# Performance work log

Measured on AMD Instinct MI355X. Metric: run time of the kernel, lower is better.

## Reference

```python
import jax, jax.numpy as jnp
import numpy as np

N = 100000   # nodes
E = 640000   # edges
G = 256      # graphs in batch
H = 128      # hidden_dim
OUT = 128    # output_dim
IN = 1       # input_dim ('standard' encoding)


def _linear_init(k, din, dout):
    # torch nn.Linear default: U(-1/sqrt(din), 1/sqrt(din)) for weight and bias
    s = 1.0 / np.sqrt(din)
    kw, kb = jax.random.split(k)
    W = jax.random.uniform(kw, (din, dout), jnp.float32, -s, s)
    b = jax.random.uniform(kb, (dout,), jnp.float32, -s, s)
    return W, b


def setup_inputs() -> dict:
    key = jax.random.key(0)
    ks = jax.random.split(key, 10)
    x = jax.random.normal(ks[0], (N, IN), jnp.float32)
    edge_index = jax.random.randint(ks[1], (2, E), 0, N, dtype=jnp.int64)
    batch = jnp.sort(jax.random.randint(ks[2], (N,), 0, G, dtype=jnp.int64))
    inp = {"x": x, "edge_index": edge_index, "batch": batch}
    dims_in = [IN, H, H]  # layer 0 takes input_dim, rest take hidden_dim
    i = 3
    for l, din in enumerate(dims_in):
        inp[f"W1_{l}"], inp[f"b1_{l}"] = _linear_init(ks[i], din, H); i += 1
        inp[f"W2_{l}"], inp[f"b2_{l}"] = _linear_init(ks[i], H, H); i += 1
    inp["Wfc"], inp["bfc"] = _linear_init(ks[i], H, OUT)
    return inp


def reference(x, edge_index, batch,
              W1_0, b1_0, W2_0, b2_0,
              W1_1, b1_1, W2_1, b2_1,
              W1_2, b1_2, W2_2, b2_2,
              Wfc, bfc):
    src, dst = edge_index[0], edge_index[1]

    def gin_conv(h, W1, b1, W2, b2):
        # GINConv, eps=0: out = MLP(h + sum_{j->i} h_j)
        agg = jax.ops.segment_sum(h[src], dst, num_segments=N)  # scatter-add messages
        z = h + agg
        return jnp.maximum(z @ W1 + b1, 0.0) @ W2 + b2

    h = gin_conv(x, W1_0, b1_0, W2_0, b2_0)
    h = gin_conv(h, W1_1, b1_1, W2_1, b2_1)
    h = gin_conv(h, W1_2, b1_2, W2_2, b2_2)
    pooled = jax.ops.segment_sum(h, batch, num_segments=G)  # global_add_pool -> [G, H]
    return pooled @ Wfc + bfc  # [G, OUT]
```

## Files before the change

### kernel.cpp

```cpp
#include <hip/hip_runtime.h>

#define HH 128
#define GG 256
#define CAP 32
#define PSPLIT 16

using f32x4  = __attribute__((ext_vector_type(4))) float;
using bf16x4 = __attribute__((ext_vector_type(4))) __bf16;
using bf16x8 = __attribute__((ext_vector_type(8))) __bf16;

static __device__ __forceinline__ float bf2f(unsigned int u) {
    unsigned int x = u << 16;
    return __builtin_bit_cast(float, x);
}
static __device__ __forceinline__ unsigned short f2bf(float f) {
    __bf16 b = (__bf16)f;
    return __builtin_bit_cast(unsigned short, b);
}

__global__ __launch_bounds__(256) void prep_k(
    int* __restrict__ cnt, float* __restrict__ pooled, int n,
    const float* __restrict__ Wa, const float* __restrict__ Wb,
    const float* __restrict__ Wc, const float* __restrict__ Wd,
    const float* __restrict__ We, __bf16* __restrict__ Wp,
    const int* __restrict__ batch, int* __restrict__ bound, int zb)
{
    const int t = threadIdx.x, b = blockIdx.x;
    if (b < zb) {
        const int i = b * 256 + t;
        if (i < n) cnt[i] = 0;
        if (i < GG * HH) pooled[i] = 0.f;
    } else if (b < zb + 40) {
        const int which = b - zb;
        const int mat = which >> 3;
        const float* W = (mat == 0) ? Wa : (mat == 1) ? Wb : (mat == 2) ? Wc
                       : (mat == 3) ? Wd : We;
        const int slot = (which & 7) * 256 + t;
        const int frag = slot >> 6, lane = slot & 63;
        const int mb = frag >> 2, kb = frag & 3;
        const int col = mb * 16 + (lane & 15);
        const int k0  = kb * 32 + (lane >> 4) * 8;
        bf16x8 v;
        #pragma unroll
        for (int j = 0; j < 8; ++j) v[j] = (__bf16)W[(k0 + j) * HH + col];
        *(bf16x8*)&Wp[(size_t)mat * 16384 + slot * 8] = v;
    } else {
        const int g = t;
        int lo = 0, hi = n;
        while (lo < hi) { int m = (lo + hi) >> 1; if (batch[m] < g) lo = m + 1; else hi = m; }
        bound[g] = lo;
        if (g == 0) bound[GG] = n;
    }
}

__global__ __launch_bounds__(256) void fill_k(const int* __restrict__ src,
                                              const int* __restrict__ dst,
                                              int* __restrict__ cnt,
                                              int* __restrict__ slotbuf, int ne)
{
    int e = blockIdx.x * 256 + threadIdx.x;
    if (e < ne) {
        const int d = dst[e];
        const int off = atomicAdd(&cnt[d], 1);
        if (off < CAP) slotbuf[d * CAP + off] = src[e];
    }
}

__global__ __launch_bounds__(256) void l0_k(
    const float* __restrict__ x,
    const int* __restrict__ cnt, const int* __restrict__ slotbuf,
    const float* __restrict__ W1, const float* __restrict__ b1,
    const __bf16* __restrict__ Wp2, const float* __restrict__ b2,
    unsigned short* __restrict__ hout, int n)
{
    __shared__ __bf16 Wl[16384];
    __shared__ unsigned short tt[4][4096];
    __shared__ float b1l[HH], b2l[HH], w1l[HH];

    const int t    = threadIdx.x;
    const int lane = t & 63, wv = t >> 6;
    const int l16  = lane & 15, lq = lane >> 4;
    const int r0    = blockIdx.x * 128 + wv * 32;
    const int nodeA = r0 + l16, nodeB = r0 + 16 + l16;
    const int rowA  = min(nodeA, n - 1), rowB = min(nodeB, n - 1);
    const int swz   = (l16 & 7) << 4;

    #pragma unroll
    for (int i = 0; i < 8; ++i)
        *(int4*)&Wl[(i * 256 + t) * 8] = *(const int4*)&Wp2[(i * 256 + t) * 8];
    if (t < HH) { b2l[t] = b2[t]; b1l[t] = b1[t]; w1l[t] = W1[t]; }

    float sA, sB;
    {
        float s0 = x[rowA], s1 = 0.f, s2 = 0.f, s3 = 0.f;
        const int dA = min(cnt[rowA], CAP);
        const int* sp = &slotbuf[rowA * CAP];
        for (int j = 0; j < dA; j += 4) {
            const int i1 = min(j + 1, dA - 1), i2 = min(j + 2, dA - 1), i3 = min(j + 3, dA - 1);
            const float v0 = x[sp[j]],  v1 = x[sp[i1]];
            const float v2 = x[sp[i2]], v3 = x[sp[i3]];
            s0 += v0;
            s1 += (j + 1 < dA) ? v1 : 0.f;
            s2 += (j + 2 < dA) ? v2 : 0.f;
            s3 += (j + 3 < dA) ? v3 : 0.f;
        }
        sA = (s0 + s1) + (s2 + s3);
        s0 = x[rowB]; s1 = s2 = s3 = 0.f;
        const int dB = min(cnt[rowB], CAP);
        const int* sq = &slotbuf[rowB * CAP];
        for (int j = 0; j < dB; j += 4) {
            const int i1 = min(j + 1, dB - 1), i2 = min(j + 2, dB - 1), i3 = min(j + 3, dB - 1);
            const float v0 = x[sq[j]],  v1 = x[sq[i1]];
            const float v2 = x[sq[i2]], v3 = x[sq[i3]];
            s0 += v0;
            s1 += (j + 1 < dB) ? v1 : 0.f;
            s2 += (j + 2 < dB) ? v2 : 0.f;
            s3 += (j + 3 < dB) ? v3 : 0.f;
        }
        sB = (s0 + s1) + (s2 + s3);
    }
    __syncthreads();

    char* tl = (char*)tt[wv];
    #pragma unroll
    for (int mt = 0; mt < 8; ++mt) {
        const f32x4 w  = *(const f32x4*)&w1l[mt * 16 + lq * 4];
        const f32x4 bb = *(const f32x4*)&b1l[mt * 16 + lq * 4];
        bf16x4 pa, pb;
        #pragma unroll
        for (int r = 0; r < 4; ++r) {
            pa[r] = (__bf16)fmaxf(fmaf(sA, w[r], bb[r]), 0.f);
            pb[r] = (__bf16)fmaxf(fmaf(sB, w[r], bb[r]), 0.f);
        }
        *(bf16x4*)(tl + ((l16 * 256 + mt * 32 + lq * 8) ^ swz)) = pa;
        *(bf16x4*)(tl + (((16 + l16) * 256 + mt * 32 + lq * 8) ^ swz)) = pb;
    }
    __syncthreads();

    bf16x8 tfA[4], tfB[4];
    #pragma unroll
    for (int kb = 0; kb < 4; ++kb) {
        tfA[kb] = *(const bf16x8*)(tl + ((l16 * 256 + kb * 64 + lq * 16) ^ swz));
        tfB[kb] = *(const bf16x8*)(tl + (((16 + l16) * 256 + kb * 64 + lq * 16) ^ swz));
    }
    f32x4 a2A[8], a2B[8];
    #pragma unroll
    for (int mb = 0; mb < 8; ++mb) {
        const f32x4 bb = *(const f32x4*)&b2l[mb * 16 + lq * 4];
        a2A[mb] = bb; a2B[mb] = bb;
    }
    #pragma unroll
    for (int mb = 0; mb < 8; ++mb)
        #pragma unroll
        for (int kb = 0; kb < 4; ++kb) {
            const bf16x8 wf = *(const bf16x8*)&Wl[((mb * 4 + kb) * 64 + lane) * 8];
            a2A[mb] = __builtin_amdgcn_mfma_f32_16x16x32_bf16(wf, tfA[kb], a2A[mb], 0, 0, 0);
            a2B[mb] = __builtin_amdgcn_mfma_f32_16x16x32_bf16(wf, tfB[kb], a2B[mb], 0, 0, 0);
        }
    if (nodeA < n) {
        #pragma unroll
        for (int mb = 0; mb < 8; ++mb) {
            bf16x4 p;
            #pragma unroll
            for (int r = 0; r < 4; ++r) p[r] = (__bf16)a2A[mb][r];
            *(bf16x4*)&hout[(size_t)nodeA * HH + mb * 16 + lq * 4] = p;
        }
    }
    if (nodeB < n) {
        #pragma unroll
        for (int mb = 0; mb < 8; ++mb) {
            bf16x4 p;
            #pragma unroll
            for (int r = 0; r < 4; ++r) p[r] = (__bf16)a2B[mb][r];
            *(bf16x4*)&hout[(size_t)nodeB * HH + mb * 16 + lq * 4] = p;
        }
    }
}

static __device__ __forceinline__ void agg_body(
    const unsigned short* __restrict__ h, const int* __restrict__ cnt,
    const int* __restrict__ slotbuf, unsigned short* __restrict__ z, int n)
{
    const int wave = (blockIdx.x * 256 + threadIdx.x) >> 6;
    const int lane = threadIdx.x & 63;
    const int half = lane >> 5, sl = lane & 31;
    const int nw   = (gridDim.x * 256) >> 6;
    const int npairs = (n + 1) >> 1;
    const uint2* h8 = (const uint2*)h;
    uint2* z8 = (uint2*)z;

    for (int pr = wave; pr < npairs; pr += nw) {
        const int node = min(2 * pr + half, n - 1);
        const int deg = min(cnt[node], CAP);
        const int* sp = &slotbuf[node * CAP];
        const uint2 su = h8[(size_t)node * 32 + sl];
        float a0 = bf2f(su.x & 0xffff), a1 = bf2f(su.x >> 16);
        float a2 = bf2f(su.y & 0xffff), a3 = bf2f(su.y >> 16);
        float b0 = 0.f, b1 = 0.f, b2 = 0.f, b3 = 0.f;
        float c0 = 0.f, c1 = 0.f, c2 = 0.f, c3 = 0.f;
        float d0 = 0.f, d1 = 0.f, d2 = 0.f, d3 = 0.f;
        for (int j = 0; j < deg; j += 4) {
            const int i1 = min(j + 1, deg - 1), i2 = min(j + 2, deg - 1), i3 = min(j + 3, deg - 1);
            const uint2 v0 = h8[(size_t)sp[j]  * 32 + sl];
            const uint2 v1 = h8[(size_t)sp[i1] * 32 + sl];
            const uint2 v2 = h8[(size_t)sp[i2] * 32 + sl];
            const uint2 v3 = h8[(size_t)sp[i3] * 32 + sl];
            a0 += bf2f(v0.x & 0xffff); a1 += bf2f(v0.x >> 16);
            a2 += bf2f(v0.y & 0xffff); a3 += bf2f(v0.y >> 16);
            const bool m1 = (j + 1 < deg), m2 = (j + 2 < deg), m3 = (j + 3 < deg);
            b0 += m1 ? bf2f(v1.x & 0xffff) : 0.f; b1 += m1 ? bf2f(v1.x >> 16) : 0.f;
            b2 += m1 ? bf2f(v1.y & 0xffff) : 0.f; b3 += m1 ? bf2f(v1.y >> 16) : 0.f;
            c0 += m2 ? bf2f(v2.x & 0xffff) : 0.f; c1 += m2 ? bf2f(v2.x >> 16) : 0.f;
            c2 += m2 ? bf2f(v2.y & 0xffff) : 0.f; c3 += m2 ? bf2f(v2.y >> 16) : 0.f;
            d0 += m3 ? bf2f(v3.x & 0xffff) : 0.f; d1 += m3 ? bf2f(v3.x >> 16) : 0.f;
            d2 += m3 ? bf2f(v3.y & 0xffff) : 0.f; d3 += m3 ? bf2f(v3.y >> 16) : 0.f;
        }
        const float s0 = (a0 + b0) + (c0 + d0);
        const float s1 = (a1 + b1) + (c1 + d1);
        const float s2 = (a2 + b2) + (c2 + d2);
        const float s3 = (a3 + b3) + (c3 + d3);
        uint2 o;
        o.x = (unsigned int)f2bf(s0) | ((unsigned int)f2bf(s1) << 16);
        o.y = (unsigned int)f2bf(s2) | ((unsigned int)f2bf(s3) << 16);
        z8[(size_t)node * 32 + sl] = o;
    }
}
__global__ __launch_bounds__(256) void agg1_k(const unsigned short* h, const int* cnt,
                                              const int* slotbuf, unsigned short* z, int n)
{ agg_body(h, cnt, slotbuf, z, n); }
__global__ __launch_bounds__(256) void agg2_k(const unsigned short* h, const int* cnt,
                                              const int* slotbuf, unsigned short* z, int n)
{ agg_body(h, cnt, slotbuf, z, n); }

static __device__ __forceinline__ void mlp_body8(
    const unsigned short* __restrict__ z,
    const __bf16* __restrict__ Wp1, const float* __restrict__ b1,
    const __bf16* __restrict__ Wp2, const float* __restrict__ b2,
    unsigned short* __restrict__ hout, int n)
{
    __shared__ __bf16 Wl1[16384], Wl2[16384];
    __shared__ unsigned short tt[8][4096];
    __shared__ float b1l[HH], b2l[HH];

    const int t    = threadIdx.x;
    const int lane = t & 63, wv = t >> 6;
    const int l16  = lane & 15, lq = lane >> 4;
    const int r0    = blockIdx.x * 256 + wv * 32;
    const int nodeA = r0 + l16, nodeB = r0 + 16 + l16;
    const int rowA  = min(nodeA, n - 1), rowB = min(nodeB, n - 1);
    const int swz   = (l16 & 7) << 4;

    #pragma unroll
    for (int i = 0; i < 4; ++i) {
        *(int4*)&Wl1[(i * 512 + t) * 8] = *(const int4*)&Wp1[(i * 512 + t) * 8];
        *(int4*)&Wl2[(i * 512 + t) * 8] = *(const int4*)&Wp2[(i * 512 + t) * 8];
    }
    if (t < HH) b1l[t] = b1[t];
    else if (t < 2 * HH) b2l[t - HH] = b2[t - HH];

    bf16x8 zfA[4], zfB[4];
    #pragma unroll
    for (int kb = 0; kb < 4; ++kb) {
        zfA[kb] = *(const bf16x8*)&z[(size_t)rowA * HH + kb * 32 + lq * 8];
        zfB[kb] = *(const bf16x8*)&z[(size_t)rowB * HH + kb * 32 + lq * 8];
    }
    __syncthreads();

    f32x4 a1A[8], a1B[8];
    #pragma unroll
    for (int mt = 0; mt < 8; ++mt) {
        const f32x4 bb = *(const f32x4*)&b1l[mt * 16 + lq * 4];
        a1A[mt] = bb; a1B[mt] = bb;
    }
    #pragma unroll
    for (int mt = 0; mt < 8; ++mt)
        #pragma unroll
        for (int kb = 0; kb < 4; ++kb) {
            const bf16x8 wf = *(const bf16x8*)&Wl1[((mt * 4 + kb) * 64 + lane) * 8];
            a1A[mt] = __builtin_amdgcn_mfma_f32_16x16x32_bf16(wf, zfA[kb], a1A[mt], 0, 0, 0);
            a1B[mt] = __builtin_amdgcn_mfma_f32_16x16x32_bf16(wf, zfB[kb], a1B[mt], 0, 0, 0);
        }
    char* tl = (char*)tt[wv];
    #pragma unroll
    for (int mt = 0; mt < 8; ++mt) {
        bf16x4 pa, pb;
        #pragma unroll
        for (int r = 0; r < 4; ++r) {
            pa[r] = (__bf16)fmaxf(a1A[mt][r], 0.f);
            pb[r] = (__bf16)fmaxf(a1B[mt][r], 0.f);
        }
        *(bf16x4*)(tl + ((l16 * 256 + mt * 32 + lq * 8) ^ swz)) = pa;
        *(bf16x4*)(tl + (((16 + l16) * 256 + mt * 32 + lq * 8) ^ swz)) = pb;
    }
    __syncthreads();

    bf16x8 tfA[4], tfB[4];
    #pragma unroll
    for (int kb = 0; kb < 4; ++kb) {
        tfA[kb] = *(const bf16x8*)(tl + ((l16 * 256 + kb * 64 + lq * 16) ^ swz));
        tfB[kb] = *(const bf16x8*)(tl + (((16 + l16) * 256 + kb * 64 + lq * 16) ^ swz));
    }
    f32x4 a2A[8], a2B[8];
    #pragma unroll
    for (int mb = 0; mb < 8; ++mb) {
        const f32x4 bb = *(const f32x4*)&b2l[mb * 16 + lq * 4];
        a2A[mb] = bb; a2B[mb] = bb;
    }
    #pragma unroll
    for (int mb = 0; mb < 8; ++mb)
        #pragma unroll
        for (int kb = 0; kb < 4; ++kb) {
            const bf16x8 wf = *(const bf16x8*)&Wl2[((mb * 4 + kb) * 64 + lane) * 8];
            a2A[mb] = __builtin_amdgcn_mfma_f32_16x16x32_bf16(wf, tfA[kb], a2A[mb], 0, 0, 0);
            a2B[mb] = __builtin_amdgcn_mfma_f32_16x16x32_bf16(wf, tfB[kb], a2B[mb], 0, 0, 0);
        }

    if (nodeA < n) {
        #pragma unroll
        for (int mb = 0; mb < 8; ++mb) {
            bf16x4 p;
            #pragma unroll
            for (int r = 0; r < 4; ++r) p[r] = (__bf16)a2A[mb][r];
            *(bf16x4*)&hout[(size_t)nodeA * HH + mb * 16 + lq * 4] = p;
        }
    }
    if (nodeB < n) {
        #pragma unroll
        for (int mb = 0; mb < 8; ++mb) {
            bf16x4 p;
            #pragma unroll
            for (int r = 0; r < 4; ++r) p[r] = (__bf16)a2B[mb][r];
            *(bf16x4*)&hout[(size_t)nodeB * HH + mb * 16 + lq * 4] = p;
        }
    }
}

__global__ __launch_bounds__(512) void mlp1_k(const unsigned short* z,
                                              const __bf16* Wp1, const float* b1,
                                              const __bf16* Wp2, const float* b2,
                                              unsigned short* h, int n)
{ mlp_body8(z, Wp1, b1, Wp2, b2, h, n); }

__global__ __launch_bounds__(512) void mlp2_k(const unsigned short* z,
                                              const __bf16* Wp1, const float* b1,
                                              const __bf16* Wp2, const float* b2,
                                              unsigned short* h, int n)
{ mlp_body8(z, Wp1, b1, Wp2, b2, h, n); }

__global__ __launch_bounds__(64) void pool_k(const unsigned short* __restrict__ h,
                                             const int* __restrict__ bound,
                                             float* __restrict__ pooled)
{
    const int g = blockIdx.x >> 4;
    const int s = blockIdx.x & (PSPLIT - 1);
    const int t = threadIdx.x;
    const int half = t >> 5, sl = t & 31;
    const int rb = bound[g], re = bound[g + 1];
    const int len = re - rb;
    const int i0 = rb + (int)(((long)len * s) / PSPLIT);
    const int i1 = rb + (int)(((long)len * (s + 1)) / PSPLIT);
    const uint2* h8 = (const uint2*)h;

    float p0 = 0.f, p1 = 0.f, p2 = 0.f, p3 = 0.f;
    float q0 = 0.f, q1 = 0.f, q2 = 0.f, q3 = 0.f;
    int r = i0 + half;
    for (; r + 2 < i1; r += 4) {
        const uint2 a = h8[(size_t)r * 32 + sl];
        const uint2 b = h8[(size_t)(r + 2) * 32 + sl];
        p0 += bf2f(a.x & 0xffff); p1 += bf2f(a.x >> 16);
        p2 += bf2f(a.y & 0xffff); p3 += bf2f(a.y >> 16);
        q0 += bf2f(b.x & 0xffff); q1 += bf2f(b.x >> 16);
        q2 += bf2f(b.y & 0xffff); q3 += bf2f(b.y >> 16);
    }
    if (r < i1) {
        const uint2 a = h8[(size_t)r * 32 + sl];
        p0 += bf2f(a.x & 0xffff); p1 += bf2f(a.x >> 16);
        p2 += bf2f(a.y & 0xffff); p3 += bf2f(a.y >> 16);
    }
    p0 += q0; p1 += q1; p2 += q2; p3 += q3;
    if (i0 + half < i1) {
        float* p = &pooled[g * HH + sl * 4];
        unsafeAtomicAdd(p + 0, p0);
        unsafeAtomicAdd(p + 1, p1);
        unsafeAtomicAdd(p + 2, p2);
        unsafeAtomicAdd(p + 3, p3);
    }
}

__global__ __launch_bounds__(128) void fc_k(const float* __restrict__ pooled,
                                            const float* __restrict__ Wfc,
                                            const float* __restrict__ bfc,
                                            float* __restrict__ out)
{
    __shared__ float p[HH];
    const int g = blockIdx.x, k = threadIdx.x;
    p[k] = pooled[g * HH + k];
    __syncthreads();
    float acc = bfc[k];
    #pragma unroll 8
    for (int j = 0; j < HH; ++j) acc = fmaf(p[j], Wfc[j * HH + k], acc);
    out[g * HH + k] = acc;
}

extern "C" void kernel_launch(void* const* d_in, const int* in_sizes, int n_in,
                              void* d_out, int out_size, void* d_ws, size_t ws_size,
                              hipStream_t stream)
{
    const float* x     = (const float*)d_in[0];
    const int*   ei    = (const int*)d_in[1];
    const int*   batch = (const int*)d_in[2];
    const float* W1_0 = (const float*)d_in[3];
    const float* b1_0 = (const float*)d_in[4];
    const float* W2_0 = (const float*)d_in[5];
    const float* b2_0 = (const float*)d_in[6];
    const float* W1_1 = (const float*)d_in[7];
    const float* b1_1 = (const float*)d_in[8];
    const float* W2_1 = (const float*)d_in[9];
    const float* b2_1 = (const float*)d_in[10];
    const float* W1_2 = (const float*)d_in[11];
    const float* b1_2 = (const float*)d_in[12];
    const float* W2_2 = (const float*)d_in[13];
    const float* b2_2 = (const float*)d_in[14];
    const float* Wfc  = (const float*)d_in[15];
    const float* bfc  = (const float*)d_in[16];

    const int N = in_sizes[0];
    const int E = in_sizes[1] / 2;
    const int* src = ei;
    const int* dst = ei + E;

    char* p = (char*)d_ws;
    #define CARVE(ty, name, count) ty* name = (ty*)p; p += (((size_t)(count) * sizeof(ty)) + 255) & ~(size_t)255;
    CARVE(unsigned short, hA,     (size_t)N * HH)
    CARVE(unsigned short, hB,     (size_t)N * HH)
    CARVE(float,          pooled, GG * HH)
    CARVE(int,            cnt,    N)
    CARVE(int,            slotbuf,(size_t)N * CAP)
    CARVE(int,            bound,  GG + 1)
    CARVE(__bf16,         Wp,     5 * 16384)
    #undef CARVE
    float* outp = (float*)d_out;

    const int gblk  = (N + 127) / 128;
    const int gblk8 = (N + 255) / 256;
    const int zb    = (N + 255) / 256;

    prep_k<<<zb + 41, 256, 0, stream>>>(cnt, pooled, N, W2_0, W1_1, W2_1, W1_2, W2_2,
                                        Wp, batch, bound, zb);
    fill_k<<<(E + 255) / 256, 256, 0, stream>>>(src, dst, cnt, slotbuf, E);

    l0_k<<<gblk, 256, 0, stream>>>(x, cnt, slotbuf, W1_0, b1_0, Wp, b2_0, hA, N);

    agg1_k<<<2048, 256, 0, stream>>>(hA, cnt, slotbuf, hB, N);
    mlp1_k<<<gblk8, 512, 0, stream>>>(hB, Wp + 16384, b1_1, Wp + 2 * 16384, b2_1, hA, N);

    agg2_k<<<2048, 256, 0, stream>>>(hA, cnt, slotbuf, hB, N);
    mlp2_k<<<gblk8, 512, 0, stream>>>(hB, Wp + 3 * 16384, b1_2, Wp + 4 * 16384, b2_2, hA, N);

    pool_k<<<GG * PSPLIT, 64, 0, stream>>>(hA, bound, pooled);
    fc_k<<<GG, HH, 0, stream>>>(pooled, Wfc, bfc, outp);
}
```

Before: 206.2 us.

## Fuse global add pooling into final MLP epilogue with shuffle-reduced atomics

The last GIN layer's MLP kernel now accumulates its outputs straight into the pooled per-graph buffer instead of writing the hidden state to memory. When a 16-row tile lies entirely inside one graph, it reduces the tile with cross-lane shuffles and issues one atomic per column; otherwise it falls back to per-node atomics. This drops the separate pool kernel, the graph-boundary binary search in prep, and one full write and read of the N×128 bf16 hidden tensor. The cost is extra shuffles and float atomics in the MLP epilogue, and the pooled sums keep fp32 outputs without rounding them to bf16 first.

```diff
diff --git a/kernel.cpp b/kernel.cpp
--- a/kernel.cpp
+++ b/kernel.cpp
@@ -3,7 +3,6 @@
 #define HH 128
 #define GG 256
 #define CAP 32
-#define PSPLIT 16
 
 using f32x4  = __attribute__((ext_vector_type(4))) float;
 using bf16x4 = __attribute__((ext_vector_type(4))) __bf16;
@@ -22,15 +21,14 @@
     int* __restrict__ cnt, float* __restrict__ pooled, int n,
     const float* __restrict__ Wa, const float* __restrict__ Wb,
     const float* __restrict__ Wc, const float* __restrict__ Wd,
-    const float* __restrict__ We, __bf16* __restrict__ Wp,
-    const int* __restrict__ batch, int* __restrict__ bound, int zb)
+    const float* __restrict__ We, __bf16* __restrict__ Wp, int zb)
 {
     const int t = threadIdx.x, b = blockIdx.x;
     if (b < zb) {
         const int i = b * 256 + t;
         if (i < n) cnt[i] = 0;
         if (i < GG * HH) pooled[i] = 0.f;
-    } else if (b < zb + 40) {
+    } else {
         const int which = b - zb;
         const int mat = which >> 3;
         const float* W = (mat == 0) ? Wa : (mat == 1) ? Wb : (mat == 2) ? Wc
@@ -44,12 +42,6 @@
         #pragma unroll
         for (int j = 0; j < 8; ++j) v[j] = (__bf16)W[(k0 + j) * HH + col];
         *(bf16x8*)&Wp[(size_t)mat * 16384 + slot * 8] = v;
-    } else {
-        const int g = t;
-        int lo = 0, hi = n;
-        while (lo < hi) { int m = (lo + hi) >> 1; if (batch[m] < g) lo = m + 1; else hi = m; }
-        bound[g] = lo;
-        if (g == 0) bound[GG] = n;
     }
 }
 
@@ -232,11 +224,13 @@
                                               const int* slotbuf, unsigned short* z, int n)
 { agg_body(h, cnt, slotbuf, z, n); }
 
+template<int POOL>
 static __device__ __forceinline__ void mlp_body8(
     const unsigned short* __restrict__ z,
     const __bf16* __restrict__ Wp1, const float* __restrict__ b1,
     const __bf16* __restrict__ Wp2, const float* __restrict__ b2,
-    unsigned short* __restrict__ hout, int n)
+    unsigned short* __restrict__ hout,
+    const int* __restrict__ batch, float* __restrict__ pooled, int n)
 {
     __shared__ __bf16 Wl1[16384], Wl2[16384];
     __shared__ unsigned short tt[8][4096];
@@ -315,22 +309,88 @@
             a2B[mb] = __builtin_amdgcn_mfma_f32_16x16x32_bf16(wf, tfB[kb], a2B[mb], 0, 0, 0);
         }
 
-    if (nodeA < n) {
-        #pragma unroll
-        for (int mb = 0; mb < 8; ++mb) {
-            bf16x4 p;
-            #pragma unroll
-            for (int r = 0; r < 4; ++r) p[r] = (__bf16)a2A[mb][r];
-            *(bf16x4*)&hout[(size_t)nodeA * HH + mb * 16 + lq * 4] = p;
-        }
-    }
-    if (nodeB < n) {
-        #pragma unroll
-        for (int mb = 0; mb < 8; ++mb) {
-            bf16x4 p;
-            #pragma unroll
-            for (int r = 0; r < 4; ++r) p[r] = (__bf16)a2B[mb][r];
-            *(bf16x4*)&hout[(size_t)nodeB * HH + mb * 16 + lq * 4] = p;
+    if (!POOL) {
+        if (nodeA < n) {
+            #pragma unroll
+            for (int mb = 0; mb < 8; ++mb) {
+                bf16x4 p;
+                #pragma unroll
+                for (int r = 0; r < 4; ++r) p[r] = (__bf16)a2A[mb][r];
+                *(bf16x4*)&hout[(size_t)nodeA * HH + mb * 16 + lq * 4] = p;
+            }
+        }
+        if (nodeB < n) {
+            #pragma unroll
+            for (int mb = 0; mb < 8; ++mb) {
+                bf16x4 p;
+                #pragma unroll
+                for (int r = 0; r < 4; ++r) p[r] = (__bf16)a2B[mb][r];
+                *(bf16x4*)&hout[(size_t)nodeB * HH + mb * 16 + lq * 4] = p;
+            }
+        }
+    } else {
+        const bool full = (r0 + 31) < n;
+        const int gA0 = batch[min(r0,      n - 1)], gA1 = batch[min(r0 + 15, n - 1)];
+        const int gB0 = batch[min(r0 + 16, n - 1)], gB1 = batch[min(r0 + 31, n - 1)];
+        if (full && gA0 == gA1) {
+            #pragma unroll
+            for (int mb = 0; mb < 8; ++mb) {
+                f32x4 v = a2A[mb];
+                #pragma unroll
+                for (int m = 1; m < 16; m <<= 1) {
+                    v[0] += __shfl_xor(v[0], m);
+                    v[1] += __shfl_xor(v[1], m);
+                    v[2] += __shfl_xor(v[2], m);
+                    v[3] += __shfl_xor(v[3], m);
+                }
+                if (l16 == 0) {
+                    float* pp = &pooled[(size_t)gA0 * HH + mb * 16 + lq * 4];
+                    unsafeAtomicAdd(pp + 0, v[0]);
+                    unsafeAtomicAdd(pp + 1, v[1]);
+                    unsafeAtomicAdd(pp + 2, v[2]);
+                    unsafeAtomicAdd(pp + 3, v[3]);
+                }
+            }
+        } else if (nodeA < n) {
+            const int g = batch[nodeA];
+            #pragma unroll
+            for (int mb = 0; mb < 8; ++mb) {
+                float* pp = &pooled[(size_t)g * HH + mb * 16 + lq * 4];
+                unsafeAtomicAdd(pp + 0, a2A[mb][0]);
+                unsafeAtomicAdd(pp + 1, a2A[mb][1]);
+                unsafeAtomicAdd(pp + 2, a2A[mb][2]);
+                unsafeAtomicAdd(pp + 3, a2A[mb][3]);
+            }
+        }
+        if (full && gB0 == gB1) {
+            #pragma unroll
+            for (int mb = 0; mb < 8; ++mb) {
+                f32x4 v = a2B[mb];
+                #pragma unroll
+                for (int m = 1; m < 16; m <<= 1) {
+                    v[0] += __shfl_xor(v[0], m);
+                    v[1] += __shfl_xor(v[1], m);
+                    v[2] += __shfl_xor(v[2], m);
+                    v[3] += __shfl_xor(v[3], m);
+                }
+                if (l16 == 0) {
+                    float* pp = &pooled[(size_t)gB0 * HH + mb * 16 + lq * 4];
+                    unsafeAtomicAdd(pp + 0, v[0]);
+                    unsafeAtomicAdd(pp + 1, v[1]);
+                    unsafeAtomicAdd(pp + 2, v[2]);
+                    unsafeAtomicAdd(pp + 3, v[3]);
+                }
+            }
+        } else if (nodeB < n) {
+            const int g = batch[nodeB];
+            #pragma unroll
+            for (int mb = 0; mb < 8; ++mb) {
+                float* pp = &pooled[(size_t)g * HH + mb * 16 + lq * 4];
+                unsafeAtomicAdd(pp + 0, a2B[mb][0]);
+                unsafeAtomicAdd(pp + 1, a2B[mb][1]);
+                unsafeAtomicAdd(pp + 2, a2B[mb][2]);
+                unsafeAtomicAdd(pp + 3, a2B[mb][3]);
+            }
         }
     }
 }
@@ -339,53 +399,13 @@
                                               const __bf16* Wp1, const float* b1,
                                               const __bf16* Wp2, const float* b2,
                                               unsigned short* h, int n)
-{ mlp_body8(z, Wp1, b1, Wp2, b2, h, n); }
+{ mlp_body8<0>(z, Wp1, b1, Wp2, b2, h, nullptr, nullptr, n); }
 
 __global__ __launch_bounds__(512) void mlp2_k(const unsigned short* z,
                                               const __bf16* Wp1, const float* b1,
                                               const __bf16* Wp2, const float* b2,
-                                              unsigned short* h, int n)
-{ mlp_body8(z, Wp1, b1, Wp2, b2, h, n); }
-
-__global__ __launch_bounds__(64) void pool_k(const unsigned short* __restrict__ h,
-                                             const int* __restrict__ bound,
-                                             float* __restrict__ pooled)
-{
-    const int g = blockIdx.x >> 4;
-    const int s = blockIdx.x & (PSPLIT - 1);
-    const int t = threadIdx.x;
-    const int half = t >> 5, sl = t & 31;
-    const int rb = bound[g], re = bound[g + 1];
-    const int len = re - rb;
-    const int i0 = rb + (int)(((long)len * s) / PSPLIT);
-    const int i1 = rb + (int)(((long)len * (s + 1)) / PSPLIT);
-    const uint2* h8 = (const uint2*)h;
-
-    float p0 = 0.f, p1 = 0.f, p2 = 0.f, p3 = 0.f;
-    float q0 = 0.f, q1 = 0.f, q2 = 0.f, q3 = 0.f;
-    int r = i0 + half;
-    for (; r + 2 < i1; r += 4) {
-        const uint2 a = h8[(size_t)r * 32 + sl];
-        const uint2 b = h8[(size_t)(r + 2) * 32 + sl];
-        p0 += bf2f(a.x & 0xffff); p1 += bf2f(a.x >> 16);
-        p2 += bf2f(a.y & 0xffff); p3 += bf2f(a.y >> 16);
-        q0 += bf2f(b.x & 0xffff); q1 += bf2f(b.x >> 16);
-        q2 += bf2f(b.y & 0xffff); q3 += bf2f(b.y >> 16);
-    }
-    if (r < i1) {
-        const uint2 a = h8[(size_t)r * 32 + sl];
-        p0 += bf2f(a.x & 0xffff); p1 += bf2f(a.x >> 16);
-        p2 += bf2f(a.y & 0xffff); p3 += bf2f(a.y >> 16);
-    }
-    p0 += q0; p1 += q1; p2 += q2; p3 += q3;
-    if (i0 + half < i1) {
-        float* p = &pooled[g * HH + sl * 4];
-        unsafeAtomicAdd(p + 0, p0);
-        unsafeAtomicAdd(p + 1, p1);
-        unsafeAtomicAdd(p + 2, p2);
-        unsafeAtomicAdd(p + 3, p3);
-    }
-}
+                                              const int* batch, float* pooled, int n)
+{ mlp_body8<1>(z, Wp1, b1, Wp2, b2, nullptr, batch, pooled, n); }
 
 __global__ __launch_bounds__(128) void fc_k(const float* __restrict__ pooled,
                                             const float* __restrict__ Wfc,
@@ -436,7 +456,6 @@
     CARVE(float,          pooled, GG * HH)
     CARVE(int,            cnt,    N)
     CARVE(int,            slotbuf,(size_t)N * CAP)
-    CARVE(int,            bound,  GG + 1)
     CARVE(__bf16,         Wp,     5 * 16384)
     #undef CARVE
     float* outp = (float*)d_out;
@@ -445,8 +464,8 @@
     const int gblk8 = (N + 255) / 256;
     const int zb    = (N + 255) / 256;
 
-    prep_k<<<zb + 41, 256, 0, stream>>>(cnt, pooled, N, W2_0, W1_1, W2_1, W1_2, W2_2,
-                                        Wp, batch, bound, zb);
+    prep_k<<<zb + 40, 256, 0, stream>>>(cnt, pooled, N, W2_0, W1_1, W2_1, W1_2, W2_2,
+                                        Wp, zb);
     fill_k<<<(E + 255) / 256, 256, 0, stream>>>(src, dst, cnt, slotbuf, E);
 
     l0_k<<<gblk, 256, 0, stream>>>(x, cnt, slotbuf, W1_0, b1_0, Wp, b2_0, hA, N);
@@ -455,8 +474,8 @@
     mlp1_k<<<gblk8, 512, 0, stream>>>(hB, Wp + 16384, b1_1, Wp + 2 * 16384, b2_1, hA, N);
 
     agg2_k<<<2048, 256, 0, stream>>>(hA, cnt, slotbuf, hB, N);
-    mlp2_k<<<gblk8, 512, 0, stream>>>(hB, Wp + 3 * 16384, b1_2, Wp + 4 * 16384, b2_2, hA, N);
-
-    pool_k<<<GG * PSPLIT, 64, 0, stream>>>(hA, bound, pooled);
+    mlp2_k<<<gblk8, 512, 0, stream>>>(hB, Wp + 3 * 16384, b1_2, Wp + 4 * 16384, b2_2,
+                                      batch, pooled, N);
+
     fc_k<<<GG, HH, 0, stream>>>(pooled, Wfc, bfc, outp);
 }
```

Result: slower. 229.1 us (+11.1%).

## Stream MLP weights from global memory instead of staging them in LDS

Applied to the files above, without the earlier changes.

The per-layer MLP kernels no longer copy both 128x128 bf16 weight matrices and the biases into shared memory. Each wave now reads its MFMA weight fragments and biases straight from global memory, relying on L1/L2 caching. The layer-1 accumulation is fused with the ReLU and store to the per-wave LDS tile, and the layer-2 accumulation with the output write, which shrinks register arrays. Blocks drop from 512 to 256 threads with a 4-block occupancy hint. This cuts LDS from about 128KB to 32KB per block, removes the block barriers, and allows more resident blocks, at the cost of repeated global or cache weight loads per wave.

```diff
diff --git a/kernel.cpp b/kernel.cpp
--- a/kernel.cpp
+++ b/kernel.cpp
@@ -232,67 +232,50 @@
                                               const int* slotbuf, unsigned short* z, int n)
 { agg_body(h, cnt, slotbuf, z, n); }
 
-static __device__ __forceinline__ void mlp_body8(
+static __device__ __forceinline__ void mlp_body4(
     const unsigned short* __restrict__ z,
     const __bf16* __restrict__ Wp1, const float* __restrict__ b1,
     const __bf16* __restrict__ Wp2, const float* __restrict__ b2,
     unsigned short* __restrict__ hout, int n)
 {
-    __shared__ __bf16 Wl1[16384], Wl2[16384];
-    __shared__ unsigned short tt[8][4096];
-    __shared__ float b1l[HH], b2l[HH];
+    __shared__ unsigned short tt[4][4096];
 
     const int t    = threadIdx.x;
     const int lane = t & 63, wv = t >> 6;
     const int l16  = lane & 15, lq = lane >> 4;
-    const int r0    = blockIdx.x * 256 + wv * 32;
+    const int r0    = blockIdx.x * 128 + wv * 32;
     const int nodeA = r0 + l16, nodeB = r0 + 16 + l16;
     const int rowA  = min(nodeA, n - 1), rowB = min(nodeB, n - 1);
     const int swz   = (l16 & 7) << 4;
 
-    #pragma unroll
-    for (int i = 0; i < 4; ++i) {
-        *(int4*)&Wl1[(i * 512 + t) * 8] = *(const int4*)&Wp1[(i * 512 + t) * 8];
-        *(int4*)&Wl2[(i * 512 + t) * 8] = *(const int4*)&Wp2[(i * 512 + t) * 8];
-    }
-    if (t < HH) b1l[t] = b1[t];
-    else if (t < 2 * HH) b2l[t - HH] = b2[t - HH];
-
     bf16x8 zfA[4], zfB[4];
     #pragma unroll
     for (int kb = 0; kb < 4; ++kb) {
         zfA[kb] = *(const bf16x8*)&z[(size_t)rowA * HH + kb * 32 + lq * 8];
         zfB[kb] = *(const bf16x8*)&z[(size_t)rowB * HH + kb * 32 + lq * 8];
     }
-    __syncthreads();
-
-    f32x4 a1A[8], a1B[8];
+
+    char* tl = (char*)tt[wv];
+
     #pragma unroll
     for (int mt = 0; mt < 8; ++mt) {
-        const f32x4 bb = *(const f32x4*)&b1l[mt * 16 + lq * 4];
-        a1A[mt] = bb; a1B[mt] = bb;
-    }
-    #pragma unroll
-    for (int mt = 0; mt < 8; ++mt)
+        const f32x4 bb = *(const f32x4*)&b1[mt * 16 + lq * 4];
+        f32x4 aA = bb, aB = bb;
         #pragma unroll
         for (int kb = 0; kb < 4; ++kb) {
-            const bf16x8 wf = *(const bf16x8*)&Wl1[((mt * 4 + kb) * 64 + lane) * 8];
-            a1A[mt] = __builtin_amdgcn_mfma_f32_16x16x32_bf16(wf, zfA[kb], a1A[mt], 0, 0, 0);
-            a1B[mt] = __builtin_amdgcn_mfma_f32_16x16x32_bf16(wf, zfB[kb], a1B[mt], 0, 0, 0);
-        }
-    char* tl = (char*)tt[wv];
-    #pragma unroll
-    for (int mt = 0; mt < 8; ++mt) {
+            const bf16x8 wf = *(const bf16x8*)&Wp1[((mt * 4 + kb) * 64 + lane) * 8];
+            aA = __builtin_amdgcn_mfma_f32_16x16x32_bf16(wf, zfA[kb], aA, 0, 0, 0);
+            aB = __builtin_amdgcn_mfma_f32_16x16x32_bf16(wf, zfB[kb], aB, 0, 0, 0);
+        }
         bf16x4 pa, pb;
         #pragma unroll
         for (int r = 0; r < 4; ++r) {
-            pa[r] = (__bf16)fmaxf(a1A[mt][r], 0.f);
-            pb[r] = (__bf16)fmaxf(a1B[mt][r], 0.f);
+            pa[r] = (__bf16)fmaxf(aA[r], 0.f);
+            pb[r] = (__bf16)fmaxf(aB[r], 0.f);
         }
         *(bf16x4*)(tl + ((l16 * 256 + mt * 32 + lq * 8) ^ swz)) = pa;
         *(bf16x4*)(tl + (((16 + l16) * 256 + mt * 32 + lq * 8) ^ swz)) = pb;
     }
-    __syncthreads();
 
     bf16x8 tfA[4], tfB[4];
     #pragma unroll
@@ -300,52 +283,42 @@
         tfA[kb] = *(const bf16x8*)(tl + ((l16 * 256 + kb * 64 + lq * 16) ^ swz));
         tfB[kb] = *(const bf16x8*)(tl + (((16 + l16) * 256 + kb * 64 + lq * 16) ^ swz));
     }
-    f32x4 a2A[8], a2B[8];
     #pragma unroll
     for (int mb = 0; mb < 8; ++mb) {
-        const f32x4 bb = *(const f32x4*)&b2l[mb * 16 + lq * 4];
-        a2A[mb] = bb; a2B[mb] = bb;
-    }
-    #pragma unroll
-    for (int mb = 0; mb < 8; ++mb)
+        const f32x4 bb = *(const f32x4*)&b2[mb * 16 + lq * 4];
+        f32x4 aA = bb, aB = bb;
         #pragma unroll
         for (int kb = 0; kb < 4; ++kb) {
-            const bf16x8 wf = *(const bf16x8*)&Wl2[((mb * 4 + kb) * 64 + lane) * 8];
-            a2A[mb] = __builtin_amdgcn_mfma_f32_16x16x32_bf16(wf, tfA[kb], a2A[mb], 0, 0, 0);
-            a2B[mb] = __builtin_amdgcn_mfma_f32_16x16x32_bf16(wf, tfB[kb], a2B[mb], 0, 0, 0);
-        }
-
-    if (nodeA < n) {
-        #pragma unroll
-        for (int mb = 0; mb < 8; ++mb) {
+            const bf16x8 wf = *(const bf16x8*)&Wp2[((mb * 4 + kb) * 64 + lane) * 8];
+            aA = __builtin_amdgcn_mfma_f32_16x16x32_bf16(wf, tfA[kb], aA, 0, 0, 0);
+            aB = __builtin_amdgcn_mfma_f32_16x16x32_bf16(wf, tfB[kb], aB, 0, 0, 0);
+        }
+        if (nodeA < n) {
             bf16x4 p;
             #pragma unroll
-            for (int r = 0; r < 4; ++r) p[r] = (__bf16)a2A[mb][r];
+            for (int r = 0; r < 4; ++r) p[r] = (__bf16)aA[r];
             *(bf16x4*)&hout[(size_t)nodeA * HH + mb * 16 + lq * 4] = p;
         }
-    }
-    if (nodeB < n) {
-        #pragma unroll
-        for (int mb = 0; mb < 8; ++mb) {
+        if (nodeB < n) {
             bf16x4 p;
             #pragma unroll
-            for (int r = 0; r < 4; ++r) p[r] = (__bf16)a2B[mb][r];
+            for (int r = 0; r < 4; ++r) p[r] = (__bf16)aB[r];
             *(bf16x4*)&hout[(size_t)nodeB * HH + mb * 16 + lq * 4] = p;
         }
     }
 }
 
-__global__ __launch_bounds__(512) void mlp1_k(const unsigned short* z,
-                                              const __bf16* Wp1, const float* b1,
-                                              const __bf16* Wp2, const float* b2,
-                                              unsigned short* h, int n)
-{ mlp_body8(z, Wp1, b1, Wp2, b2, h, n); }
-
-__global__ __launch_bounds__(512) void mlp2_k(const unsigned short* z,
-                                              const __bf16* Wp1, const float* b1,
-                                              const __bf16* Wp2, const float* b2,
-                                              unsigned short* h, int n)
-{ mlp_body8(z, Wp1, b1, Wp2, b2, h, n); }
+__global__ __launch_bounds__(256, 4) void mlp1_k(const unsigned short* z,
+                                                 const __bf16* Wp1, const float* b1,
+                                                 const __bf16* Wp2, const float* b2,
+                                                 unsigned short* h, int n)
+{ mlp_body4(z, Wp1, b1, Wp2, b2, h, n); }
+
+__global__ __launch_bounds__(256, 4) void mlp2_k(const unsigned short* z,
+                                                 const __bf16* Wp1, const float* b1,
+                                                 const __bf16* Wp2, const float* b2,
+                                                 unsigned short* h, int n)
+{ mlp_body4(z, Wp1, b1, Wp2, b2, h, n); }
 
 __global__ __launch_bounds__(64) void pool_k(const unsigned short* __restrict__ h,
                                              const int* __restrict__ bound,
@@ -441,9 +414,8 @@
     #undef CARVE
     float* outp = (float*)d_out;
 
-    const int gblk  = (N + 127) / 128;
-    const int gblk8 = (N + 255) / 256;
-    const int zb    = (N + 255) / 256;
+    const int gblk = (N + 127) / 128;
+    const int zb   = (N + 255) / 256;
 
     prep_k<<<zb + 41, 256, 0, stream>>>(cnt, pooled, N, W2_0, W1_1, W2_1, W1_2, W2_2,
                                         Wp, batch, bound, zb);
@@ -452,10 +424,10 @@
     l0_k<<<gblk, 256, 0, stream>>>(x, cnt, slotbuf, W1_0, b1_0, Wp, b2_0, hA, N);
 
     agg1_k<<<2048, 256, 0, stream>>>(hA, cnt, slotbuf, hB, N);
-    mlp1_k<<<gblk8, 512, 0, stream>>>(hB, Wp + 16384, b1_1, Wp + 2 * 16384, b2_1, hA, N);
+    mlp1_k<<<gblk, 256, 0, stream>>>(hB, Wp + 16384, b1_1, Wp + 2 * 16384, b2_1, hA, N);
 
     agg2_k<<<2048, 256, 0, stream>>>(hA, cnt, slotbuf, hB, N);
-    mlp2_k<<<gblk8, 512, 0, stream>>>(hB, Wp + 3 * 16384, b1_2, Wp + 4 * 16384, b2_2, hA, N);
+    mlp2_k<<<gblk, 256, 0, stream>>>(hB, Wp + 3 * 16384, b1_2, Wp + 4 * 16384, b2_2, hA, N);
 
     pool_k<<<GG * PSPLIT, 64, 0, stream>>>(hA, bound, pooled);
     fc_k<<<GG, HH, 0, stream>>>(pooled, Wfc, bfc, outp);
```

New measurement: 211.7 us. +2.7%, slower.
